# Performance work log

Hardware: AMD Instinct MI355X
Metric: run time of the kernel (lower is better)

The kernel has to match this reference:

```python
import jax, jax.numpy as jnp
import numpy as np
from jax import lax

ANCHOR_BASE = np.array([
    [-37.254833, -82.50967, 53.254833, 98.50967],
    [-82.50967, -173.01933, 98.50967, 189.01933],
    [-173.01933, -354.03867, 189.01933, 370.03867],
    [-56.0, -56.0, 72.0, 72.0],
    [-120.0, -120.0, 136.0, 136.0],
    [-248.0, -248.0, 264.0, 264.0],
    [-82.50967, -37.254833, 98.50967, 53.254833],
    [-173.01933, -82.50967, 189.01933, 98.50967],
    [-354.03867, -173.01933, 370.03867, 189.01933]], dtype=np.float32)
FEAT_STRIDE = 16
IMG_H, IMG_W = 608, 800          # feature map 38x50 at stride 16
NMS_THRESH = 0.7
PRE_NMS, POST_NMS = 6000, 300
MIN_SIZE = 16.0                  # scale = 1.0


def setup_inputs() -> dict:
    key = jax.random.key(0)
    ks = jax.random.split(key, 7)
    H, W = 38, 50
    x = jax.random.normal(ks[0], (1, 512, H, W), jnp.float32)
    conv1_w = jax.random.normal(ks[1], (512, 512, 3, 3), jnp.float32) * 0.01
    conv1_b = jnp.zeros((512,), jnp.float32)
    loc_w = jax.random.normal(ks[2], (36, 512, 1, 1), jnp.float32) * 0.01
    loc_b = jnp.zeros((36,), jnp.float32)
    score_w = jax.random.normal(ks[3], (18, 512, 1, 1), jnp.float32) * 0.01
    score_b = jnp.zeros((18,), jnp.float32)
    return {"x": x, "conv1_w": conv1_w, "conv1_b": conv1_b,
            "loc_w": loc_w, "loc_b": loc_b,
            "score_w": score_w, "score_b": score_b}


def _conv(x, w, b, pad):
    y = lax.conv_general_dilated(x, w, (1, 1), pad,
                                 dimension_numbers=("NCHW", "OIHW", "NCHW"))
    return y + b[None, :, None, None]


def _make_anchors(h, w):
    ab = jnp.asarray(ANCHOR_BASE)                       # [A,4]
    yy = jnp.arange(h, dtype=jnp.float32) * FEAT_STRIDE
    xx = jnp.arange(w, dtype=jnp.float32) * FEAT_STRIDE
    sy, sx = jnp.meshgrid(yy, xx, indexing="ij")        # [h,w]
    shift = jnp.stack([sy, sx, sy, sx], axis=-1).reshape(-1, 4)  # [K,4]
    return (shift[:, None, :] + ab[None, :, :]).reshape(-1, 4)   # [K*A,4]


def _loc2bbox(anchor, loc):
    ah = anchor[:, 2] - anchor[:, 0]
    aw = anchor[:, 3] - anchor[:, 1]
    acy = anchor[:, 0] + 0.5 * ah
    acx = anchor[:, 1] + 0.5 * aw
    dy, dx, dh, dw = loc[:, 0], loc[:, 1], loc[:, 2], loc[:, 3]
    cy = dy * ah + acy
    cx = dx * aw + acx
    h = jnp.exp(dh) * ah
    w = jnp.exp(dw) * aw
    return jnp.stack([cy - 0.5 * h, cx - 0.5 * w,
                      cy + 0.5 * h, cx + 0.5 * w], axis=1)


def _iou_matrix(b):  # b: [K,4] (y1,x1,y2,x2)
    area = (b[:, 2] - b[:, 0]) * (b[:, 3] - b[:, 1])
    ty1 = jnp.maximum(b[:, None, 0], b[None, :, 0])
    tx1 = jnp.maximum(b[:, None, 1], b[None, :, 1])
    ty2 = jnp.minimum(b[:, None, 2], b[None, :, 2])
    tx2 = jnp.minimum(b[:, None, 3], b[None, :, 3])
    inter = jnp.clip(ty2 - ty1, 0) * jnp.clip(tx2 - tx1, 0)
    return inter / jnp.maximum(area[:, None] + area[None, :] - inter, 1e-9)


def _nms_keep(boxes, valid, thresh):
    # boxes already sorted by score desc; greedy suppression.
    K = boxes.shape[0]
    iou = _iou_matrix(boxes)                 # [K,K]
    idx = jnp.arange(K)

    def body(i, keep):
        sup = (iou[i] > thresh) & (idx > i) & keep[i]
        return keep & ~sup

    keep = lax.fori_loop(0, K, body, valid)
    return keep


def reference(x, conv1_w, conv1_b, loc_w, loc_b, score_w, score_b):
    H, W = x.shape[2], x.shape[3]
    A = ANCHOR_BASE.shape[0]

    h1 = jax.nn.relu(_conv(x, conv1_w, conv1_b, ((1, 1), (1, 1))))
    locs = _conv(h1, loc_w, loc_b, ((0, 0), (0, 0)))      # [1,36,H,W]
    scores = _conv(h1, score_w, score_b, ((0, 0), (0, 0)))  # [1,18,H,W]

    locs = locs.transpose(0, 2, 3, 1).reshape(-1, 4)        # [H*W*A,4]
    fg = scores.transpose(0, 2, 3, 1).reshape(H, W, A, 2)[..., 1].reshape(-1)

    anchor = _make_anchors(H, W)
    roi = _loc2bbox(anchor, locs)
    roi = jnp.stack([jnp.clip(roi[:, 0], 0, IMG_H),
                     jnp.clip(roi[:, 1], 0, IMG_W),
                     jnp.clip(roi[:, 2], 0, IMG_H),
                     jnp.clip(roi[:, 3], 0, IMG_W)], axis=1)

    hs = roi[:, 2] - roi[:, 0]
    ws = roi[:, 3] - roi[:, 1]
    valid = (hs >= MIN_SIZE) & (ws >= MIN_SIZE)
    score_f = jnp.where(valid, fg, -jnp.inf)

    top_scores, top_idx = lax.top_k(score_f, PRE_NMS)
    top_boxes = roi[top_idx]                                # [PRE_NMS,4]
    top_valid = top_scores > -jnp.inf

    keep = _nms_keep(top_boxes, top_valid, NMS_THRESH)

    # take first POST_NMS kept boxes into a fixed-shape output
    rank = jnp.cumsum(keep.astype(jnp.int32)) - 1
    dest = jnp.where(keep & (rank < POST_NMS), rank, POST_NMS)
    out = jnp.zeros((POST_NMS + 1, 4), top_boxes.dtype).at[dest].add(top_boxes)
    return out[:POST_NMS]
```

## Files before the change

### kernel.cpp

```cpp
#include <hip/hip_runtime.h>
#include <cstdint>
#include <cstddef>

typedef unsigned long long u64;

#define CIN   512
#define H     38
#define W     50
#define HW    1900
#define PH    40
#define PW    52
#define NA    17100
#define NSORT 32768
#define PRE   6000
#define POST  300
#define NW    94
#define MTS   6016
#define TOPN  6016
#define PB    8

__constant__ float c_AB[36] = {
  -37.254833f,  -82.50967f,   53.254833f,  98.50967f,
  -82.50967f,  -173.01933f,   98.50967f,  189.01933f,
 -173.01933f,  -354.03867f,  189.01933f,  370.03867f,
  -56.f, -56.f, 72.f, 72.f,
 -120.f,-120.f,136.f,136.f,
 -248.f,-248.f,264.f,264.f,
  -82.50967f,  -37.254833f,   98.50967f,  53.254833f,
 -173.01933f,  -82.50967f,   189.01933f,  98.50967f,
 -354.03867f, -173.01933f,   370.03867f, 189.01933f
};

__global__ __launch_bounds__(256) void prep_kernel(const float* __restrict__ x, float* __restrict__ xp,
                                                   const float* __restrict__ w1, float* __restrict__ wt) {
  __shared__ float tile[9][16][17];
  int b = blockIdx.x;
  if (b < 4160) {
    int idx = b * 256 + threadIdx.x;
    int c   = idx / (PH * PW);
    int rem = idx - c * (PH * PW);
    int yy  = rem / PW;
    int xx  = rem - yy * PW;
    float v = 0.f;
    if (yy >= 1 && yy <= H && xx >= 1 && xx <= W)
      v = x[(size_t)c * HW + (yy - 1) * W + (xx - 1)];
    xp[idx] = v;
  } else {
    int t2 = b - 4160;
    int o0 = (t2 & 31) * 16, i0 = (t2 >> 5) * 16;
    int tx = threadIdx.x & 15, ty = threadIdx.x >> 4;
    #pragma unroll
    for (int r = 0; r < 9; ++r)
      tile[r][tx][ty] = w1[((size_t)(o0 + ty) * CIN + (i0 + tx)) * 9 + r];
    __syncthreads();
    #pragma unroll
    for (int r = 0; r < 9; ++r)
      wt[((size_t)r * CIN + i0 + ty) * CIN + o0 + tx] = tile[r][ty][tx];
  }
}

__global__ __launch_bounds__(256) void conv_gemm_kernel(const float* __restrict__ wt, const float* __restrict__ xp,
                                                        float* __restrict__ part) {
  __shared__ __align__(16) float As[16][64];
  __shared__ __align__(16) float Bs[16][64];
  const int tid   = threadIdx.x;
  const int obase = blockIdx.x * 64;
  const int pbase = blockIdx.y * 64;
  const int split = blockIdx.z;
  const int kbeg = split * 1536, kend = kbeg + 1536;
  const int krow = tid >> 4;
  const int c4   = (tid & 15) * 4;
  const int to   = (tid & 15) * 4;
  const int tp   = (tid >> 4) * 4;
  float acc[4][4] = {};
  float av[4], bv[4];

  auto loadAB = [&](int k0) {
    int k = k0 + krow;
    const float* ap = &wt[(size_t)k * CIN + obase + c4];
    av[0] = ap[0]; av[1] = ap[1]; av[2] = ap[2]; av[3] = ap[3];
    int r = k >> 9;
    int i = k & 511;
    int ky = r / 3, kx = r - ky * 3;
    const float* xpi = &xp[(size_t)i * (PH * PW)];
    #pragma unroll
    for (int j = 0; j < 4; ++j) {
      int p = pbase + c4 + j;
      float v = 0.f;
      if (p < HW) {
        int y = p / W, xx = p - y * W;
        v = xpi[(y + ky) * PW + xx + kx];
      }
      bv[j] = v;
    }
  };

  loadAB(kbeg);
  for (int k0 = kbeg; k0 < kend; k0 += 16) {
    __syncthreads();
    *(float4*)&As[krow][c4] = make_float4(av[0], av[1], av[2], av[3]);
    *(float4*)&Bs[krow][c4] = make_float4(bv[0], bv[1], bv[2], bv[3]);
    __syncthreads();
    if (k0 + 16 < kend) loadAB(k0 + 16);
    #pragma unroll
    for (int kk = 0; kk < 16; ++kk) {
      float4 a4 = *(const float4*)&As[kk][to];
      float4 b4 = *(const float4*)&Bs[kk][tp];
      float ar[4] = {a4.x, a4.y, a4.z, a4.w};
      float br[4] = {b4.x, b4.y, b4.z, b4.w};
      #pragma unroll
      for (int ii = 0; ii < 4; ++ii)
        #pragma unroll
        for (int jj = 0; jj < 4; ++jj)
          acc[ii][jj] += ar[ii] * br[jj];
    }
  }
  float* dst = part + (size_t)split * CIN * HW;
  #pragma unroll
  for (int ii = 0; ii < 4; ++ii) {
    int o = obase + to + ii;
    int p = pbase + tp;
    float* rowp = dst + (size_t)o * HW;
    if (p + 3 < HW) {
      *(float4*)&rowp[p] = make_float4(acc[ii][0], acc[ii][1], acc[ii][2], acc[ii][3]);
    } else {
      #pragma unroll
      for (int jj = 0; jj < 4; ++jj) if (p + jj < HW) rowp[p + jj] = acc[ii][jj];
    }
  }
}

__global__ __launch_bounds__(256) void relu_heads_kernel(const float* __restrict__ part, const float* __restrict__ b1,
                                                         const float* __restrict__ lw, const float* __restrict__ sw,
                                                         const float* __restrict__ lb, const float* __restrict__ sb,
                                                         float* __restrict__ c2) {
  __shared__ float h1c[CIN][PB];
  const int tid = threadIdx.x;
  const int p0  = blockIdx.x * PB;
  for (int e = tid; e < CIN * PB; e += 256) {
    int o  = e >> 3;
    int pp = e & (PB - 1);
    int p  = p0 + pp;
    float v = 0.f;
    if (p < HW) {
      size_t idx = (size_t)o * HW + p;
      v = part[idx] + part[(size_t)CIN * HW + idx] + part[(size_t)2 * CIN * HW + idx] + b1[o];
      v = v > 0.f ? v : 0.f;
    }
    h1c[o][pp] = v;
  }
  __syncthreads();
  for (int u = tid; u < 54 * PB; u += 256) {
    int o  = u >> 3;
    int pp = u & (PB - 1);
    int p  = p0 + pp;
    const float* __restrict__ ap = (o < 36) ? (lw + (size_t)o * CIN) : (sw + (size_t)(o - 36) * CIN);
    float acc = 0.f;
    #pragma unroll 1
    for (int g = 0; g < CIN; g += 16) {
      float4 a0 = *(const float4*)(ap + g);
      float4 a1 = *(const float4*)(ap + g + 4);
      float4 a2 = *(const float4*)(ap + g + 8);
      float4 a3 = *(const float4*)(ap + g + 12);
      acc += a0.x * h1c[g +  0][pp];  acc += a0.y * h1c[g +  1][pp];
      acc += a0.z * h1c[g +  2][pp];  acc += a0.w * h1c[g +  3][pp];
      acc += a1.x * h1c[g +  4][pp];  acc += a1.y * h1c[g +  5][pp];
      acc += a1.z * h1c[g +  6][pp];  acc += a1.w * h1c[g +  7][pp];
      acc += a2.x * h1c[g +  8][pp];  acc += a2.y * h1c[g +  9][pp];
      acc += a2.z * h1c[g + 10][pp];  acc += a2.w * h1c[g + 11][pp];
      acc += a3.x * h1c[g + 12][pp];  acc += a3.y * h1c[g + 13][pp];
      acc += a3.z * h1c[g + 14][pp];  acc += a3.w * h1c[g + 15][pp];
    }
    if (p < HW) {
      float bias = (o < 36) ? lb[o] : sb[o - 36];
      c2[(size_t)o * HW + p] = acc + bias;
    }
  }
}

__global__ __launch_bounds__(256) void decode_sort_kernel(const float* __restrict__ c2, float* __restrict__ roi,
                                                          u64* __restrict__ keys) {
  __shared__ u64 s[2048];
  const int tid = threadIdx.x;
  const int nbase = blockIdx.x * 2048;
  for (int i = tid; i < 2048; i += 256) {
    int n = nbase + i;
    u64 key;
    if (n >= NA) {
      key = ~0ull;
    } else {
      unsigned p = (unsigned)n / 9u;
      unsigned a = (unsigned)n - p * 9u;
      unsigned y = p / 50u;
      unsigned xu = p - y * 50u;
      float dy = c2[(a * 4 + 0) * HW + p];
      float dx = c2[(a * 4 + 1) * HW + p];
      float dh = c2[(a * 4 + 2) * HW + p];
      float dw = c2[(a * 4 + 3) * HW + p];
      float fg = c2[(37 + a * 2) * HW + p];
      float sy = (float)(y * 16u), sx = (float)(xu * 16u);
      float ay1 = sy + c_AB[a * 4 + 0], ax1 = sx + c_AB[a * 4 + 1];
      float ay2 = sy + c_AB[a * 4 + 2], ax2 = sx + c_AB[a * 4 + 3];
      float ahh = ay2 - ay1, aww = ax2 - ax1;
      float acy = ay1 + 0.5f * ahh, acx = ax1 + 0.5f * aww;
      float cy = dy * ahh + acy, cx = dx * aww + acx;
      float hh = expf(dh) * ahh, ww = expf(dw) * aww;
      float y1 = cy - 0.5f * hh, x1 = cx - 0.5f * ww;
      float y2 = cy + 0.5f * hh, x2 = cx + 0.5f * ww;
      y1 = fminf(fmaxf(y1, 0.f), 608.f); x1 = fminf(fmaxf(x1, 0.f), 800.f);
      y2 = fminf(fmaxf(y2, 0.f), 608.f); x2 = fminf(fmaxf(x2, 0.f), 800.f);
      *(float4*)&roi[(size_t)n * 4] = make_float4(y1, x1, y2, x2);
      bool valid = ((y2 - y1) >= 16.f) && ((x2 - x1) >= 16.f);
      float sc = valid ? fg : -__builtin_huge_valf();
      unsigned m = __float_as_uint(sc);
      m = (m & 0x80000000u) ? ~m : (m | 0x80000000u);
      unsigned km = ~m;
      key = ((u64)km << 32) | (unsigned)n;
    }
    s[i] = key;
  }
  __syncthreads();
  for (int k = 2; k <= 2048; k <<= 1) {
    for (int j = k >> 1; j > 0; j >>= 1) {
      for (int i = tid; i < 2048; i += 256) {
        int l = i ^ j;
        if (l > i) {
          u64 xa = s[i], xb = s[l];
          bool up = ((i & k) == 0);
          if ((xa > xb) == up) { s[i] = xb; s[l] = xa; }
        }
      }
      __syncthreads();
    }
  }
  for (int i = tid; i < 2048; i += 256) keys[nbase + i] = s[i];
}

__device__ inline void merge_path(const u64* __restrict__ A, int nA, const u64* __restrict__ B, int nB,
                                  u64* __restrict__ dst, int d0, int cnt, int outLimit) {
  if (d0 >= outLimit || d0 >= nA + nB) return;
  int lo = d0 > nB ? d0 - nB : 0;
  int hi = d0 < nA ? d0 : nA;
  while (lo < hi) {
    int mid = (lo + hi) >> 1;
    if (A[mid] <= B[d0 - 1 - mid]) lo = mid + 1; else hi = mid;
  }
  int i = lo, j = d0 - lo;
  int end = d0 + cnt;
  if (end > nA + nB) end = nA + nB;
  if (end > outLimit) end = outLimit;
  for (int q = d0; q < end; ++q) {
    u64 v;
    if (i < nA && (j >= nB || A[i] <= B[j])) v = A[i++]; else v = B[j++];
    dst[q] = v;
  }
}

__global__ __launch_bounds__(256) void merge4_kernel(const u64* __restrict__ keys, u64* __restrict__ tmp) {
  __shared__ u64 M01[4096];
  __shared__ u64 M23[4096];
  const int tid = threadIdx.x;
  const u64* c = keys + (size_t)blockIdx.x * 8192;
  merge_path(c,        2048, c + 2048, 2048, M01, tid * 16, 16, 4096);
  merge_path(c + 4096, 2048, c + 6144, 2048, M23, tid * 16, 16, 4096);
  __syncthreads();
  merge_path(M01, 4096, M23, 4096, tmp + (size_t)blockIdx.x * TOPN, tid * 24, 24, TOPN);
}

__global__ __launch_bounds__(256) void mergefinal_gather_kernel(const u64* __restrict__ tmp,
                                                                const float* __restrict__ roi,
                                                                float* __restrict__ tb, float* __restrict__ areaArr,
                                                                u64* __restrict__ valw) {
  __shared__ u64 L0[TOPN];
  __shared__ u64 L1[TOPN];
  __shared__ u64 F[TOPN];
  const int tid = threadIdx.x;
  merge_path(tmp,            TOPN, tmp + TOPN,     TOPN, L0, tid * 24, 24, TOPN);
  merge_path(tmp + 2 * TOPN, TOPN, tmp + 3 * TOPN, TOPN, L1, tid * 24, 24, TOPN);
  __syncthreads();
  merge_path(L0, TOPN, L1, TOPN, F, tid * 24, 24, TOPN);
  __syncthreads();
  for (int j0 = 0; j0 < TOPN; j0 += 256) {
    int j = j0 + tid;
    u64 key = F[j];
    bool valid = (j < PRE) && ((unsigned)(key >> 32) < 0xFF800000u);
    if (j < PRE) {
      unsigned idx = (unsigned)key;
      float4 bx = *(const float4*)&roi[(size_t)idx * 4];
      *(float4*)&tb[(size_t)j * 4] = bx;
      areaArr[j] = (bx.z - bx.x) * (bx.w - bx.y);
    }
    u64 mask = __ballot(valid);
    if ((tid & 63) == 0) {
      int wi = j >> 6;
      if (wi < NW) valw[wi] = mask;
    }
  }
}

__global__ __launch_bounds__(256) void mask_kernel(const float* __restrict__ tb, const float* __restrict__ areaArr,
                                                   u64* __restrict__ MT) {
  int linear = blockIdx.x * 256 + threadIdx.x;
  if (linear >= NW * PRE) return;
  int w = linear / PRE;
  int i = linear - w * PRE;
  u64 bits = 0;
  int jbase = w * 64;
  if (jbase + 63 > i) {
    float4 bi = *(const float4*)&tb[(size_t)i * 4];
    float ai = areaArr[i];
    int jend = jbase + 64; if (jend > PRE) jend = PRE;
    int jst = jbase > i + 1 ? jbase : i + 1;
    for (int j = jst; j < jend; ++j) {
      float4 bj = *(const float4*)&tb[(size_t)j * 4];
      float ty1 = fmaxf(bi.x, bj.x);
      float tx1 = fmaxf(bi.y, bj.y);
      float ty2 = fminf(bi.z, bj.z);
      float tx2 = fminf(bi.w, bj.w);
      float ih = ty2 - ty1; if (ih < 0.f) ih = 0.f;
      float iw = tx2 - tx1; if (iw < 0.f) iw = 0.f;
      float inter = ih * iw;
      float denom = ai + areaArr[j] - inter;
      if (denom < 1e-9f) denom = 1e-9f;
      if (inter / denom > 0.7f) bits |= (1ull << (j - jbase));
    }
  }
  MT[(size_t)w * MTS + i] = bits;
}

__device__ inline u64 shfl_u64(u64 v, int src) {
  int lo = __shfl((int)(unsigned)(v & 0xffffffffull), src, 64);
  int hi = __shfl((int)(unsigned)(v >> 32), src, 64);
  return ((u64)(unsigned)hi << 32) | (unsigned)lo;
}
__device__ inline u64 shfl_u64_xor(u64 v, int m) {
  int lo = __shfl_xor((int)(unsigned)(v & 0xffffffffull), m, 64);
  int hi = __shfl_xor((int)(unsigned)(v >> 32), m, 64);
  return ((u64)(unsigned)hi << 32) | (unsigned)lo;
}

__global__ __launch_bounds__(64) void nms_scan_kernel(const u64* __restrict__ MT, const u64* __restrict__ valw,
                                                      const float* __restrict__ tb, float* __restrict__ out) {
  __shared__ int keepids[POST];
  const int lane = threadIdx.x;
  int kept = 0;
  bool done = false;
  for (int g = 0; g < NW && !done; ++g) {
    const u64* __restrict__ rowg = MT + (size_t)g * MTS;
    u64 rem = 0;
    for (int base = 0; base < kept; base += 64) {
      int kidx = base + lane;
      u64 v = (kidx < kept) ? rowg[keepids[kidx]] : 0ull;
      rem |= v;
    }
    #pragma unroll
    for (int s = 32; s > 0; s >>= 1) rem |= shfl_u64_xor(rem, s);
    int row = g * 64 + lane;
    u64 cur = (row < PRE) ? rowg[row] : 0ull;
    u64 remaining = valw[g] & ~rem;
    while (remaining) {
      int c = __builtin_ctzll(remaining);
      if (lane == 0) keepids[kept] = g * 64 + c;
      ++kept;
      if (kept >= POST) { done = true; break; }
      u64 cw = shfl_u64(cur, c);
      u64 above = (c == 63) ? 0ull : (~0ull << (c + 1));
      remaining = remaining & ~cw & above;
    }
  }
  __syncthreads();
  int kmax = kept < POST ? kept : POST;
  for (int rr = lane; rr < kmax; rr += 64) {
    float4 b = *(const float4*)&tb[(size_t)keepids[rr] * 4];
    *(float4*)&out[(size_t)rr * 4] = b;
  }
}

extern "C" void kernel_launch(void* const* d_in, const int* in_sizes, int n_in,
                              void* d_out, int out_size, void* d_ws, size_t ws_size,
                              hipStream_t stream) {
  (void)in_sizes; (void)n_in; (void)ws_size;
  const float* x  = (const float*)d_in[0];
  const float* w1 = (const float*)d_in[1];
  const float* b1 = (const float*)d_in[2];
  const float* lw = (const float*)d_in[3];
  const float* lb = (const float*)d_in[4];
  const float* sw = (const float*)d_in[5];
  const float* sb = (const float*)d_in[6];
  float* out = (float*)d_out;

  char* wp = (char*)d_ws;
  auto alloc = [&](size_t b) -> void* { void* p = wp; wp += (b + 255) & ~(size_t)255; return p; };
  float* xp      = (float*)alloc((size_t)CIN * PH * PW * 4);
  float* wt      = (float*)alloc((size_t)4608 * CIN * 4);
  float* part    = (float*)alloc((size_t)3 * CIN * HW * 4);
  float* c2      = (float*)alloc((size_t)64 * HW * 4);
  float* roi     = (float*)alloc((size_t)NA * 4 * 4);
  u64*   keys    = (u64*)alloc((size_t)NSORT * 8);
  u64*   tmp     = (u64*)alloc((size_t)4 * TOPN * 8);
  float* tb      = (float*)alloc((size_t)PRE * 4 * 4);
  float* areaArr = (float*)alloc((size_t)PRE * 4);
  u64*   valw    = (u64*)alloc((size_t)NW * 8);
  u64*   MT      = (u64*)alloc((size_t)NW * MTS * 8);

  hipMemsetAsync(d_out, 0, (size_t)out_size * 4, stream);

  prep_kernel<<<5184, 256, 0, stream>>>(x, xp, w1, wt);
  conv_gemm_kernel<<<dim3(8, 30, 3), 256, 0, stream>>>(wt, xp, part);
  relu_heads_kernel<<<(HW + PB - 1) / PB, 256, 0, stream>>>(part, b1, lw, sw, lb, sb, c2);
  decode_sort_kernel<<<16, 256, 0, stream>>>(c2, roi, keys);
  merge4_kernel<<<4, 256, 0, stream>>>(keys, tmp);
  mergefinal_gather_kernel<<<1, 256, 0, stream>>>(tmp, roi, tb, areaArr, valw);
  mask_kernel<<<(NW * PRE + 255) / 256, 256, 0, stream>>>(tb, areaArr, MT);
  nms_scan_kernel<<<1, 64, 0, stream>>>(MT, valw, tb, out);
}
```

Before: 462.6 us.

## Read conv input directly from global memory instead of staging through LDS

Removes the shared-memory B tile in the implicit-GEMM conv. Each thread now reads its four input pixels straight from global memory (through cache) with precomputed offsets, and the K loop is split by kernel column so the ky/kx index math is hoisted out. This drops one LDS store and the per-element division in the B loads. In exchange it issues many scattered, non-prefetched global loads inside the inner FMA loop, and each value is re-read by the 16 threads that share a pixel column.

```diff
diff --git a/kernel.cpp b/kernel.cpp
--- a/kernel.cpp
+++ b/kernel.cpp
@@ -62,59 +62,66 @@
 __global__ __launch_bounds__(256) void conv_gemm_kernel(const float* __restrict__ wt, const float* __restrict__ xp,
                                                         float* __restrict__ part) {
   __shared__ __align__(16) float As[16][64];
-  __shared__ __align__(16) float Bs[16][64];
   const int tid   = threadIdx.x;
   const int obase = blockIdx.x * 64;
   const int pbase = blockIdx.y * 64;
   const int split = blockIdx.z;
-  const int kbeg = split * 1536, kend = kbeg + 1536;
   const int krow = tid >> 4;
   const int c4   = (tid & 15) * 4;
   const int to   = (tid & 15) * 4;
   const int tp   = (tid >> 4) * 4;
-  float acc[4][4] = {};
-  float av[4], bv[4];
-
-  auto loadAB = [&](int k0) {
-    int k = k0 + krow;
-    const float* ap = &wt[(size_t)k * CIN + obase + c4];
-    av[0] = ap[0]; av[1] = ap[1]; av[2] = ap[2]; av[3] = ap[3];
-    int r = k >> 9;
-    int i = k & 511;
-    int ky = r / 3, kx = r - ky * 3;
-    const float* xpi = &xp[(size_t)i * (PH * PW)];
+
+  int boff[4];
+  {
+    int p0 = pbase + tp;
     #pragma unroll
     for (int j = 0; j < 4; ++j) {
-      int p = pbase + c4 + j;
-      float v = 0.f;
-      if (p < HW) {
-        int y = p / W, xx = p - y * W;
-        v = xpi[(y + ky) * PW + xx + kx];
+      int p = p0 + j; if (p >= HW) p = HW - 1;
+      int y = p / 50, xx = p - y * 50;
+      boff[j] = y * PW + xx;
+    }
+  }
+
+  float acc[4][4] = {};
+  float av[4];
+
+  #pragma unroll 1
+  for (int kx = 0; kx < 3; ++kx) {
+    const int kchunk = split * 1536 + kx * 512;
+    const float* __restrict__ xpc = xp + split * PW + kx;
+    int i0 = boff[0], i1 = boff[1], i2 = boff[2], i3 = boff[3];
+
+    {
+      int k = kchunk + krow;
+      const float* ap = &wt[(size_t)k * CIN + obase + c4];
+      av[0] = ap[0]; av[1] = ap[1]; av[2] = ap[2]; av[3] = ap[3];
+    }
+    #pragma unroll 1
+    for (int k0 = kchunk; k0 < kchunk + 512; k0 += 16) {
+      __syncthreads();
+      *(float4*)&As[krow][c4] = make_float4(av[0], av[1], av[2], av[3]);
+      __syncthreads();
+      if (k0 + 16 < kchunk + 512) {
+        int k = k0 + 16 + krow;
+        const float* ap = &wt[(size_t)k * CIN + obase + c4];
+        av[0] = ap[0]; av[1] = ap[1]; av[2] = ap[2]; av[3] = ap[3];
       }
-      bv[j] = v;
-    }
-  };
-
-  loadAB(kbeg);
-  for (int k0 = kbeg; k0 < kend; k0 += 16) {
-    __syncthreads();
-    *(float4*)&As[krow][c4] = make_float4(av[0], av[1], av[2], av[3]);
-    *(float4*)&Bs[krow][c4] = make_float4(bv[0], bv[1], bv[2], bv[3]);
-    __syncthreads();
-    if (k0 + 16 < kend) loadAB(k0 + 16);
-    #pragma unroll
-    for (int kk = 0; kk < 16; ++kk) {
-      float4 a4 = *(const float4*)&As[kk][to];
-      float4 b4 = *(const float4*)&Bs[kk][tp];
-      float ar[4] = {a4.x, a4.y, a4.z, a4.w};
-      float br[4] = {b4.x, b4.y, b4.z, b4.w};
       #pragma unroll
-      for (int ii = 0; ii < 4; ++ii)
+      for (int kk = 0; kk < 16; ++kk) {
+        float4 a4 = *(const float4*)&As[kk][to];
+        float br[4];
+        br[0] = xpc[i0]; br[1] = xpc[i1]; br[2] = xpc[i2]; br[3] = xpc[i3];
+        float ar[4] = {a4.x, a4.y, a4.z, a4.w};
         #pragma unroll
-        for (int jj = 0; jj < 4; ++jj)
-          acc[ii][jj] += ar[ii] * br[jj];
-    }
-  }
+        for (int ii = 0; ii < 4; ++ii)
+          #pragma unroll
+          for (int jj = 0; jj < 4; ++jj)
+            acc[ii][jj] += ar[ii] * br[jj];
+        i0 += PH * PW; i1 += PH * PW; i2 += PH * PW; i3 += PH * PW;
+      }
+    }
+  }
+
   float* dst = part + (size_t)split * CIN * HW;
   #pragma unroll
   for (int ii = 0; ii < 4; ++ii) {
```

Result: slower. 542.0 us (+17.2%).
